# Performance work log

Measured on AMD Instinct MI355X. Metric: run time of the kernel, lower is better.

## Reference

```python
import jax, jax.numpy as jnp
import numpy as np
from jax import lax

B, S, T = 32, 128, 128
V_SRC, V_TGT, E, U = 32000, 32000, 128, 256


def _lstm(xs, h0, c0, Wx, Wh, b):
    # xs: [T, B, F]; Keras gate order i, f, g(candidate), o
    def step(carry, x):
        h, c = carry
        z = x @ Wx + h @ Wh + b
        i, f, g, o = jnp.split(z, 4, axis=-1)
        c = jax.nn.sigmoid(f) * c + jax.nn.sigmoid(i) * jnp.tanh(g)
        h = jax.nn.sigmoid(o) * jnp.tanh(c)
        return (h, c), h
    (h, c), hs = lax.scan(step, (h0, c0), xs)
    return hs, h, c


def setup_inputs() -> dict:
    key = jax.random.key(0)
    ks = jax.random.split(key, 20)
    p = lambda k, shp: (jax.random.normal(k, shp, dtype=jnp.float32) * 0.02)
    return {
        "src": jax.random.randint(ks[0], (B, S), 0, V_SRC),
        "tgt": jax.random.randint(ks[1], (B, T), 0, V_TGT),
        "enc_emb": p(ks[2], (V_SRC, E)),
        "enc_Wx": p(ks[3], (E, 4 * U)),
        "enc_Wh": p(ks[4], (U, 4 * U)),
        "enc_b": jnp.zeros((4 * U,), jnp.float32),
        "dec_emb": p(ks[5], (V_TGT, E)),
        "dec_Wx": p(ks[6], (U + E, 4 * U)),
        "dec_Wh": p(ks[7], (U, 4 * U)),
        "dec_b": jnp.zeros((4 * U,), jnp.float32),
        "att_W1": p(ks[8], (U, U)),
        "att_b1": jnp.zeros((U,), jnp.float32),
        "att_W2": p(ks[9], (U, U)),
        "att_b2": jnp.zeros((U,), jnp.float32),
        "att_V": p(ks[10], (U, 1)),
        "att_bV": jnp.zeros((1,), jnp.float32),
        "fc_W": p(ks[11], (U, V_TGT)),
        "fc_b": jnp.zeros((V_TGT,), jnp.float32),
    }


def reference(src, tgt, enc_emb, enc_Wx, enc_Wh, enc_b, dec_emb, dec_Wx, dec_Wh,
              dec_b, att_W1, att_b1, att_W2, att_b2, att_V, att_bV, fc_W, fc_b):
    # ---- encoder ----
    enc_x = enc_emb[src]                                  # [B,S,E]
    enc_hs, h, c = _lstm(enc_x.transpose(1, 0, 2),
                         jnp.zeros((B, U), enc_Wx.dtype),
                         jnp.zeros((B, U), enc_Wx.dtype),
                         enc_Wx, enc_Wh, enc_b)
    enc_out = enc_hs.transpose(1, 0, 2)                   # [B,S,U]
    keys = enc_out @ att_W2 + att_b2                      # [B,S,U] (hoisted, same math)

    # ---- decoder (faithful: step 0 uses tgt[:,0]; step t>=1 uses tgt[:,t-1]) ----
    dec_tokens = jnp.concatenate([tgt[:, :1], tgt[:, :-1]], axis=1)  # [B,T]
    dec_x = dec_emb[dec_tokens].transpose(1, 0, 2)        # [T,B,E]

    def step(carry, x_emb):
        h, c = carry
        q = (h @ att_W1 + att_b1)[:, None, :]             # [B,1,U]
        score = jnp.tanh(q + keys) @ att_V + att_bV       # [B,S,1]
        attn = jax.nn.softmax(score, axis=1)
        ctx = jnp.sum(attn * enc_out, axis=1)             # [B,U]
        xin = jnp.concatenate([ctx, x_emb], axis=-1)      # [B,U+E]
        z = xin @ dec_Wx + h @ dec_Wh + dec_b
        i, f, g, o = jnp.split(z, 4, axis=-1)
        c = jax.nn.sigmoid(f) * c + jax.nn.sigmoid(i) * jnp.tanh(g)
        h = jax.nn.sigmoid(o) * jnp.tanh(c)
        probs = jax.nn.softmax(h @ fc_W + fc_b, axis=-1)  # [B,V]
        return (h, c), probs

    _, out = lax.scan(step, (h, c), dec_x)                # [T,B,V]
    return out.transpose(1, 0, 2)                         # [B,T,V]
```

## Files before the change

kernel.cpp:

```cpp
#include <hip/hip_runtime.h>
#include <hip/hip_bf16.h>
#include <hip/hip_fp16.h>
#include <cstdint>
#include <cstddef>

#define B_ 32
#define S_ 128
#define T_ 128
#define E_ 128
#define U_ 256
#define V_ 32000
#define G4 1024
#define TV 4096000

typedef __attribute__((ext_vector_type(8))) short short8_t;
typedef __attribute__((ext_vector_type(8))) unsigned short ushort8_t;
typedef __attribute__((ext_vector_type(4))) float f32x4;
typedef unsigned long long u64;

static __device__ __forceinline__ unsigned short f2bf(float x) {
  union { float f; unsigned int u; } v; v.f = x;
  unsigned int r = (v.u + 0x7fffu + ((v.u >> 16) & 1u)) >> 16;
  return (unsigned short)r;
}
static __device__ __forceinline__ float bf2f(unsigned short u) {
  return __uint_as_float(((unsigned)u) << 16);
}
static __device__ __forceinline__ float sigmoidf_(float x) {
  return 1.0f / (1.0f + __expf(-x));
}
static __device__ __forceinline__ float tanhf_(float x) {
  float e = __expf(2.0f * x);
  return 1.0f - 2.0f / (e + 1.0f);
}

static __device__ __forceinline__ unsigned int f2e5(float x) {
  __half h = __float2half(x);
  __half_raw hr = *(__half_raw*)&h;
  unsigned int u = hr.x;
  unsigned int r = (u + 0x7Fu + ((u >> 8) & 1u)) >> 8;
  return r & 0xFFu;
}

static __device__ __forceinline__ unsigned pk2(float a, float b) {
  auto h = __builtin_amdgcn_cvt_pkrtz(a, b);
  return __builtin_bit_cast(unsigned, h);
}
#define SEL01 0x05000400u
#define SEL23 0x07000600u
static __device__ __forceinline__ unsigned e5pair(unsigned w, unsigned sel) {
  return __builtin_amdgcn_perm(w, 0u, sel);
}
static __device__ __forceinline__ float dot2(unsigned a, unsigned b, float c) {
  float d;
  asm("v_dot2_f32_f16 %0, %1, %2, %3" : "=v"(d) : "v"(a), "v"(b), "v"(c));
  return d;
}
static __device__ __forceinline__ unsigned pkadd(unsigned a, unsigned b) {
  unsigned d; asm("v_pk_add_f16 %0, %1, %2" : "=v"(d) : "v"(a), "v"(b)); return d;
}
static __device__ __forceinline__ unsigned pkmul(unsigned a, unsigned b) {
  unsigned d; asm("v_pk_mul_f16 %0, %1, %2" : "=v"(d) : "v"(a), "v"(b)); return d;
}
static __device__ __forceinline__ unsigned pkfma(unsigned a, unsigned b, unsigned c) {
  unsigned d; asm("v_pk_fma_f16 %0, %1, %2, %3" : "=v"(d) : "v"(a), "v"(b), "v"(c)); return d;
}
static __device__ __forceinline__ unsigned pkmax(unsigned a, unsigned b) {
  unsigned d; asm("v_pk_max_f16 %0, %1, %2" : "=v"(d) : "v"(a), "v"(b)); return d;
}
static __device__ __forceinline__ unsigned pkmin(unsigned a, unsigned b) {
  unsigned d; asm("v_pk_min_f16 %0, %1, %2" : "=v"(d) : "v"(a), "v"(b)); return d;
}

static __device__ __forceinline__ void gload_lds16(const void* g, void* l) {
  __builtin_amdgcn_global_load_lds(
      (const __attribute__((address_space(1))) unsigned int*)g,
      (__attribute__((address_space(3))) unsigned int*)l, 16, 0, 0);
}

static __device__ __forceinline__ void pub64u(u64* p, unsigned val, unsigned tag) {
  u64 v = ((u64)tag << 32) | (u64)val;
  __hip_atomic_store(p, v, __ATOMIC_RELAXED, __HIP_MEMORY_SCOPE_AGENT);
}
static __device__ __forceinline__ u64 ld64(const u64* p) {
  return __hip_atomic_load(p, __ATOMIC_RELAXED, __HIP_MEMORY_SCOPE_AGENT);
}

__global__ __launch_bounds__(256) void k_prep(
    const int* __restrict__ src, const int* __restrict__ tgt,
    const float* __restrict__ enc_emb, const float* __restrict__ enc_Wx,
    const float* __restrict__ enc_b,
    const float* __restrict__ dec_emb, const float* __restrict__ dec_Wx,
    const float* __restrict__ dec_b,
    float* __restrict__ Xe, float* __restrict__ Xd,
    const float* __restrict__ fcW, unsigned short* __restrict__ fcWt)
{
  __shared__ float shmem[64 * 65];
  int wg = blockIdx.x;
  int tid = threadIdx.x;

  if (wg >= 1024) {
    int bid = wg - 1024;
    int n0 = (bid % 500) * 64, k0 = (bid / 500) * 64;
    for (int i = 0; i < 16; ++i) {
      int lin = i * 256 + tid;
      int k = lin >> 6, n = lin & 63;
      shmem[k * 65 + n] = fcW[(size_t)(k0 + k) * V_ + n0 + n];
    }
    __syncthreads();
    for (int i = 0; i < 16; ++i) {
      int lin = i * 256 + tid;
      int n = lin >> 6, k = lin & 63;
      fcWt[(size_t)(n0 + n) * 256 + k0 + k] = f2bf(shmem[k * 65 + n]);
    }
    return;
  }

  bool is_dec = (wg >= 512);
  int r0 = (is_dec ? (wg - 512) : wg) * 8;
  const float* emb  = is_dec ? dec_emb : enc_emb;
  const float* W    = is_dec ? (dec_Wx + (size_t)U_ * G4) : enc_Wx;
  const float* bias = is_dec ? dec_b : enc_b;
  float* Xout = is_dec ? Xd : Xe;

  for (int i = 0; i < 4; ++i) {
    int lin = i * 256 + tid;
    int rr = lin >> 7, k = lin & 127;
    int r = r0 + rr;
    int b = r & 31, st = r >> 5;
    int tok;
// ... 90 lines not shown
      c_reg = c;
      float h = sigmoidf_(z[3]) * tanhf_(c);
      h_reg = h;
      enc_out[((size_t)(b * S_ + s)) * U_ + gc] = h;
      if (s < S_ - 1) {
        float hx = __shfl_xor(h, 1);
        if (!(r & 1))
          pub64u(&hpubE[((size_t)((s + 1) & 1) * 32 + b) * 128 + g * 16 + (r >> 1)],
                 pk2(h, hx), (unsigned)(s + 1));
      }
    }
    if (s < S_ - 1 && tid < 128) {
      const u64* p = &hpubE[((size_t)((s + 1) & 1) * 32 + b) * 128 + tid];
      u64 v = ld64(p);
      while ((unsigned)(v >> 32) < (unsigned)(s + 1)) { __builtin_amdgcn_s_sleep(1); v = ld64(p); }
      h2[tid] = (unsigned)v;
    }
    __syncthreads();
  }
  if (tid < 32) {
    h_state[b * U_ + g * 32 + tid] = h_reg;
    c_state[b * U_ + g * 32 + tid] = c_reg;
  }
}

__global__ __launch_bounds__(256) void k_keys(
    const float* __restrict__ enc_out, const float* __restrict__ W2,
    const float* __restrict__ b2,
    unsigned char* __restrict__ keys8, unsigned char* __restrict__ eo8T)
{
  __shared__ float x_l[8][U_];
  int wg = blockIdx.x, tid = threadIdx.x;
  int r0 = wg * 8;
  for (int i = 0; i < 8; ++i) x_l[i][tid] = enc_out[(size_t)(r0 + i) * U_ + tid];
  __syncthreads();
  float acc[8];
  #pragma unroll
  for (int rr = 0; rr < 8; ++rr) acc[rr] = 0.f;
  for (int k = 0; k < U_; ++k) {
    float w = W2[(size_t)k * U_ + tid];
    #pragma unroll
    for (int rr = 0; rr < 8; ++rr) acc[rr] += x_l[rr][k] * w;
  }
  float bb = b2[tid];
  #pragma unroll
  for (int rr = 0; rr < 8; ++rr) {
    int r = r0 + rr;
    keys8[(size_t)r * U_ + tid] = (unsigned char)f2e5(acc[rr] + bb);
    int bI = r >> 7, sI = r & 127;
    eo8T[((size_t)bI * U_ + tid) * S_ + sI] = (unsigned char)f2e5(x_l[rr][tid]);
  }
}

__global__ __launch_bounds__(1024) void k_decoder(
    const float* __restrict__ Xd, const float* __restrict__ dec_Wx,
    const float* __restrict__ Wh,
    const float* __restrict__ W1, const float* __restrict__ b1,
    const float* __restrict__ attV, const float* __restrict__ attbV,
    const unsigned char* __restrict__ keys8, const unsigned char* __restrict__ eo8T,
    const float* __restrict__ h0, const float* __restrict__ c0,
    unsigned short* __restrict__ Hbf,
    u64* __restrict__ hpub2 )
{
  __shared__ unsigned int WxU[64 * 128];
  __shared__ unsigned int WhU[64 * 128];
  __shared__ unsigned int W1U[64 * 256];
  __shared__ float scr_q[4 * 256];
  __shared__ float scr_c[4 * 256];
  __shared__ float scr_z[8 * 128];
  __shared__ unsigned int q2[160];
  __shared__ unsigned int aV2[160];
  __shared__ unsigned int h2[128];
  __shared__ unsigned int ctx2[128];
  __shared__ unsigned int esc2[64];
  __shared__ float escw[16];
  __shared__ float b1_l[256];

  int bid = blockIdx.x, tid = threadIdx.x;
  int b = bid & 31, g = bid >> 5;
  int lane = tid & 63, wid = tid >> 6;

  for (int idx = tid; idx < 64 * 128; idx += 1024) {
    int k4 = idx >> 7, c = idx & 127;
    int gc = (c >> 5) * 256 + g * 32 + (c & 31);
    unsigned wx = 0, wh = 0;
    #pragma unroll
    for (int i = 0; i < 4; ++i) {
      int k = 4 * k4 + i;
      wx |= f2e5(dec_Wx[(size_t)k * G4 + gc]) << (8 * i);
      wh |= f2e5(Wh[(size_t)k * G4 + gc]) << (8 * i);
    }
    WxU[k4 * 128 + c] = wx;
    WhU[k4 * 128 + c] = wh;
  }
  for (int idx = tid; idx < 64 * 256; idx += 1024) {
    int k4 = idx >> 8, u = idx & 255;
    unsigned w = 0;
    #pragma unroll
    for (int i = 0; i < 4; ++i)
      w |= f2e5(W1[(size_t)(4 * k4 + i) * U_ + u]) << (8 * i);
    W1U[k4 * 256 + u] = w;
  }
  if (tid < 128) {
    int p = tid;
    aV2[(p >> 4) * 20 + (p & 15)] = pk2(attV[2 * p], attV[2 * p + 1]);
  }
  if (tid < 256) b1_l[tid] = b1[tid];
  float bV = attbV[0];
  float c_reg = 0.f, h_reg = 0.f;
  if (tid < 32) {
    h_reg = h0[b * U_ + g * 32 + tid];
    c_reg = c0[b * U_ + g * 32 + tid];
  }
  __syncthreads();

  if (tid < 32) {
    float hx = __shfl_xor(h_reg, 1);
    if (!(tid & 1))
      pub64u(&hpub2[((size_t)0 * 32 + b) * 128 + g * 16 + (tid >> 1)], pk2(h_reg, hx), 1u);
  }
  if (tid < 128) {
    const u64* hp = &hpub2[((size_t)0 * 32 + b) * 128 + tid];
    u64 vh = ld64(hp);
    while ((unsigned)(vh >> 32) < 1u) { __builtin_amdgcn_s_sleep(1); vh = ld64(hp); }
    h2[tid] = (unsigned)vh;
  }
  __syncthreads();

  const unsigned NEG1 = pk2(-1.f, -1.f), POS1 = pk2(1.f, 1.f);
  const unsigned C1 = pk2(-0.333333333f, -0.333333333f);
  const unsigned C2 = pk2(0.133333333f, 0.133333333f);
  const unsigned C3 = pk2(-0.053968254f, -0.053968254f);

  const unsigned char* kb = keys8 + (size_t)b * S_ * U_;
  const unsigned char* eb = eo8T + (size_t)b * U_ * S_;

  for (int t = 0; t < T_; ++t) {
    float xd0 = 0.f, xd1 = 0.f, xd2 = 0.f, xd3 = 0.f;
    if (tid < 32) {
      const float* xd = Xd + (size_t)(t * B_ + b) * G4 + g * 32 + tid;
      xd0 = xd[0]; xd1 = xd[256]; xd2 = xd[512]; xd3 = xd[768];
    }

    int sI = tid >> 3, uo = tid & 7;
    int uI = tid & 255, sq = tid >> 8;
    uint4 kA, kB, eA, eB;
    {
      const uint4* kp = (const uint4*)(kb + (size_t)sI * U_ + uo * 32);
      kA = kp[0]; kB = kp[1];
      const uint4* ep = (const uint4*)(eb + (size_t)uI * S_ + sq * 32);
      eA = ep[0]; eB = ep[1];
    }
    {
      int c = tid & 255, kq = tid >> 8;
      const unsigned* wp = &W1U[(kq * 16) * 256 + c];
      const unsigned* hh = &h2[kq * 32];
      float qa = 0.f, qb = 0.f;
      #pragma unroll
      for (int j = 0; j < 16; ++j) {
        unsigned w = wp[j * 256];
        qa = dot2(e5pair(w, SEL01), hh[2 * j], qa);
        qb = dot2(e5pair(w, SEL23), hh[2 * j + 1], qb);
      }
      scr_q[kq * 256 + c] = qa + qb;
    }
    __syncthreads();

    if (tid < 128) {
      int u0 = 2 * tid;
      float q0 = scr_q[u0] + scr_q[256 + u0] + scr_q[512 + u0] + scr_q[768 + u0] + b1_l[u0];
      float q1 = scr_q[u0 + 1] + scr_q[256 + u0 + 1] + scr_q[512 + u0 + 1] + scr_q[768 + u0 + 1] + b1_l[u0 + 1];
      q2[(tid >> 4) * 20 + (tid & 15)] = pk2(q0, q1);
    }
    __syncthreads();

    {
      unsigned kw[8] = {kA.x, kA.y, kA.z, kA.w, kB.x, kB.y, kB.z, kB.w};
      const unsigned* qq = &q2[uo * 20];
      const unsigned* vv = &aV2[uo * 20];
      float a0 = 0.f, a1 = 0.f;
      #pragma unroll
      for (int j = 0; j < 8; ++j) {
        unsigned w = kw[j];
        unsigned x0 = pkadd(e5pair(w, SEL01), qq[2 * j]);
        unsigned x1 = pkadd(e5pair(w, SEL23), qq[2 * j + 1]);
        x0 = pkmin(pkmax(x0, NEG1), POS1);
        x1 = pkmin(pkmax(x1, NEG1), POS1);
        unsigned s0_ = pkmul(x0, x0), s1_ = pkmul(x1, x1);
        unsigned t0 = pkfma(s0_, C3, C2), t1 = pkfma(s1_, C3, C2);
        t0 = pkfma(s0_, t0, C1); t1 = pkfma(s1_, t1, C1);
        unsigned th0 = pkfma(pkmul(x0, s0_), t0, x0);
        unsigned th1 = pkfma(pkmul(x1, s1_), t1, x1);
        a0 = dot2(th0, vv[2 * j], a0);
        a1 = dot2(th1, vv[2 * j + 1], a1);
      }
      float a = a0 + a1;
      a += __shfl_xor(a, 1); a += __shfl_xor(a, 2); a += __shfl_xor(a, 4);
      float ea = __expf(a + bV);
      float ep = __shfl_xor(ea, 8);
      if (uo == 0 && !(sI & 1)) esc2[sI >> 1] = pk2(ea, ep);
      float dsum = ea;
      dsum += __shfl_xor(dsum, 8); dsum += __shfl_xor(dsum, 16); dsum += __shfl_xor(dsum, 32);
      if (lane == 0) escw[wid] = dsum;
    }
    __syncthreads();

    {
      unsigned ewv[8] = {eA.x, eA.y, eA.z, eA.w, eB.x, eB.y, eB.z, eB.w};
      const unsigned* e2 = &esc2[sq * 16];
      float c0a = 0.f, c1a = 0.f;
      #pragma unroll
      for (int j = 0; j < 8; ++j) {
        unsigned w = ewv[j];
        c0a = dot2(e5pair(w, SEL01), e2[2 * j], c0a);
        c1a = dot2(e5pair(w, SEL23), e2[2 * j + 1], c1a);
      }
      scr_c[sq * 256 + uI] = c0a + c1a;
    }
    __syncthreads();

    if (tid < 128) {
      int u0 = 2 * tid;
      float ca = scr_c[u0] + scr_c[256 + u0] + scr_c[512 + u0] + scr_c[768 + u0];
      float cb = scr_c[u0 + 1] + scr_c[256 + u0 + 1] + scr_c[512 + u0 + 1] + scr_c[768 + u0 + 1];
      ctx2[tid] = pk2(ca, cb);
    }
    __syncthreads();

    {
      float d = ((escw[0] + escw[1]) + (escw[2] + escw[3])) +
                ((escw[4] + escw[5]) + (escw[6] + escw[7])) +
                ((escw[8] + escw[9]) + (escw[10] + escw[11])) +
                ((escw[12] + escw[13]) + (escw[14] + escw[15]));
      float dinv = 1.0f / d;
      int c = tid & 127, k8 = tid >> 7;
      const unsigned* wxp = &WxU[(k8 * 8) * 128 + c];
      const unsigned* whp = &WhU[(k8 * 8) * 128 + c];
      const unsigned* cc = &ctx2[k8 * 16];
      const unsigned* hh = &h2[k8 * 16];
      float zx0 = 0.f, zx1 = 0.f, zh0 = 0.f, zh1 = 0.f;
      #pragma unroll
      for (int j = 0; j < 8; ++j) {
        unsigned wx = wxp[j * 128], wh = whp[j * 128];
        zx0 = dot2(e5pair(wx, SEL01), cc[2 * j], zx0);
        zx1 = dot2(e5pair(wx, SEL23), cc[2 * j + 1], zx1);
        zh0 = dot2(e5pair(wh, SEL01), hh[2 * j], zh0);
        zh1 = dot2(e5pair(wh, SEL23), hh[2 * j + 1], zh1);
      }
      scr_z[k8 * 128 + c] = (zh0 + zh1) + (zx0 + zx1) * dinv;
    }
    __syncthreads();

    if (tid < 32) {
      int r = tid, gc = g * 32 + r;
      float z[4] = {xd0, xd1, xd2, xd3};
      #pragma unroll
      for (int q = 0; q < 4; ++q) {
        int c = q * 32 + r;
        #pragma unroll
        for (int k8 = 0; k8 < 8; ++k8) z[q] += scr_z[k8 * 128 + c];
      }
      float c = sigmoidf_(z[1]) * c_reg + sigmoidf_(z[0]) * tanhf_(z[2]);
      c_reg = c;
      float h = sigmoidf_(z[3]) * tanhf_(c);
      h_reg = h;
      Hbf[(size_t)(t * B_ + b) * U_ + gc] = f2bf(h);
      if (t < T_ - 1) {
        int par1 = (t + 1) & 1;
        float hx = __shfl_xor(h, 1);
        if (!(r & 1))
          pub64u(&hpub2[((size_t)par1 * 32 + b) * 128 + g * 16 + (r >> 1)],
                 pk2(h, hx), (unsigned)(t + 2));
      }
    }
    if (t < T_ - 1 && tid < 128) {
      int par1 = (t + 1) & 1;
      unsigned tag2 = (unsigned)(t + 2);
      const u64* hp = &hpub2[((size_t)par1 * 32 + b) * 128 + tid];
      u64 vh = ld64(hp);
      while ((unsigned)(vh >> 32) < tag2) { __builtin_amdgcn_s_sleep(1); vh = ld64(hp); }
      h2[tid] = (unsigned)vh;
    }
    __syncthreads();
  }
}

__global__ __launch_bounds__(256) void k_fc(
    const unsigned short* __restrict__ Hbf, const unsigned short* __restrict__ fcWt,
    const float* __restrict__ fcb, float* __restrict__ out,
    unsigned short* __restrict__ expv,
    float* __restrict__ rs_part)
{
  __shared__ uint4 Al[128 * 8];
  __shared__ uint4 Bl[128 * 8];
  __shared__ float rsum_l[128][2];

  int bid = blockIdx.x, tid = threadIdx.x;
  int nt = bid >> 5, mt = bid & 31;
  int m0 = mt * 128, n0 = nt * 128;
  int lane = tid & 63, wave = tid >> 6;
  int wm = (wave >> 1) * 64, wn = (wave & 1) * 64;
  int g = lane >> 4, r15 = lane & 15;

  f32x4 acc[4][4];
  f32x4 zero = {0.f, 0.f, 0.f, 0.f};
  #pragma unroll
  for (int mi = 0; mi < 4; ++mi)
    #pragma unroll
    for (int ni = 0; ni < 4; ++ni) acc[mi][ni] = zero;

  const unsigned short* Ag = Hbf  + (size_t)m0 * 256;
  const unsigned short* Bg = fcWt + (size_t)n0 * 256;

  int lin0 = tid;
  for (int kt = 0; kt < 4; ++kt) {
    int kk = kt * 64;
    #pragma unroll
    for (int blk = 0; blk < 4; ++blk) {
      int lin = blk * 256 + lin0;
      int row = lin >> 3, kq = lin & 7;
      int kqs = kq ^ (row & 7);
      gload_lds16(Ag + (size_t)row * 256 + kk + kqs * 8,
                  &Al[blk * 256 + wave * 64]);
      gload_lds16(Bg + (size_t)row * 256 + kk + kqs * 8,
                  &Bl[blk * 256 + wave * 64]);
    }
    __syncthreads();
    #pragma unroll
    for (int kk2 = 0; kk2 < 2; ++kk2) {
      short8_t a[4], bfr[4];
      #pragma unroll
      for (int mi = 0; mi < 4; ++mi) {
        int row = wm + mi * 16 + r15;
        a[mi] = *(const short8_t*)&Al[row * 8 + ((kk2 * 4 + g) ^ (row & 7))];
      }
      #pragma unroll
      for (int ni = 0; ni < 4; ++ni) {
        int row = wn + ni * 16 + r15;
        bfr[ni] = *(const short8_t*)&Bl[row * 8 + ((kk2 * 4 + g) ^ (row & 7))];
      }
      #pragma unroll
      for (int mi = 0; mi < 4; ++mi)
        #pragma unroll
        for (int ni = 0; ni < 4; ++ni)
          acc[mi][ni] = __builtin_amdgcn_mfma_f32_16x16x32_bf16(a[mi], bfr[ni], acc[mi][ni], 0, 0, 0);
    }
    __syncthreads();
  }

  float fcb_l[4];
  #pragma unroll
  for (int ni = 0; ni < 4; ++ni) fcb_l[ni] = fcb[n0 + wn + ni * 16 + r15];

  #pragma unroll
  for (int mi = 0; mi < 4; ++mi) {
    #pragma unroll
    for (int jj = 0; jj < 4; ++jj) {
      int rloc = wm + mi * 16 + g * 4 + jj;
      int grow = m0 + rloc;
      int bb = grow & 31, tt = grow >> 5;
      size_t obase = (size_t)bb * TV + (size_t)tt * V_;
      float s = 0.f;
      if (expv) {
        #pragma unroll
        for (int ni = 0; ni < 4; ++ni) {
          float v = __expf(acc[mi][ni][jj] + fcb_l[ni]);
          unsigned short us = f2bf(v);
          expv[obase + n0 + wn + ni * 16 + r15] = us;
          s += bf2f(us);
        }
      } else {
        #pragma unroll
        for (int ni = 0; ni < 4; ++ni) {
          float v = __expf(acc[mi][ni][jj] + fcb_l[ni]);
          out[obase + n0 + wn + ni * 16 + r15] = v;
          s += v;
        }
      }
      s += __shfl_xor(s, 1); s += __shfl_xor(s, 2);
      s += __shfl_xor(s, 4); s += __shfl_xor(s, 8);
      if (r15 == 0) rsum_l[rloc][wave & 1] = s;
    }
  }
  __syncthreads();
  if (tid < 128)
    rs_part[(size_t)nt * 4096 + m0 + tid] = rsum_l[tid][0] + rsum_l[tid][1];
}

__global__ __launch_bounds__(256) void k_rowsum(
    const float* __restrict__ rs_part, float* __restrict__ row_inv)
{
  int gidx = blockIdx.x * 256 + threadIdx.x;
  float s = 0.f;
  for (int nt = 0; nt < 250; ++nt) s += rs_part[(size_t)nt * 4096 + gidx];
  row_inv[gidx] = 1.0f / s;
}

__global__ __launch_bounds__(256) void k_norm_bf16(
    const unsigned short* __restrict__ expv, float* __restrict__ out,
    const float* __restrict__ row_inv)
{
  const long total = 16384000;
  long stride = (long)gridDim.x * 256;
  for (long i = (long)blockIdx.x * 256 + threadIdx.x; i < total; i += stride) {
    long flat = i * 8;
    int bb = (int)(flat / TV);
    int rem = (int)(flat % TV);
    int tt = rem / V_;
    float sc = row_inv[tt * 32 + bb];
    ushort8_t v = *(const ushort8_t*)&expv[flat];
    float4 o0, o1;
    o0.x = bf2f(v[0]) * sc; o0.y = bf2f(v[1]) * sc;
    o0.z = bf2f(v[2]) * sc; o0.w = bf2f(v[3]) * sc;
    o1.x = bf2f(v[4]) * sc; o1.y = bf2f(v[5]) * sc;
    o1.z = bf2f(v[6]) * sc; o1.w = bf2f(v[7]) * sc;
    *(float4*)&out[flat] = o0;
    *(float4*)&out[flat + 4] = o1;
  }
}

__global__ __launch_bounds__(256) void k_norm(
    float4* __restrict__ out4, const float* __restrict__ row_inv)
{
  const long total = 32768000;
  long stride = (long)gridDim.x * 256;
  for (long i = (long)blockIdx.x * 256 + threadIdx.x; i < total; i += stride) {
    long flat = i * 4;
    int bb = (int)(flat / TV);
    int rem = (int)(flat % TV);
    int tt = rem / V_;
    float sc = row_inv[tt * 32 + bb];
    float4 v = out4[i];
    v.x *= sc; v.y *= sc; v.z *= sc; v.w *= sc;
    out4[i] = v;
  }
}

extern "C" void kernel_launch(void* const* d_in, const int* in_sizes, int n_in,
                              void* d_out, int out_size, void* d_ws, size_t ws_size,
                              hipStream_t stream) {
  (void)in_sizes; (void)n_in; (void)out_size;
  const int*   src     = (const int*)d_in[0];
  const int*   tgt     = (const int*)d_in[1];
  const float* enc_emb = (const float*)d_in[2];
  const float* enc_Wx  = (const float*)d_in[3];
  const float* enc_Wh  = (const float*)d_in[4];
  const float* enc_b   = (const float*)d_in[5];
  const float* dec_emb = (const float*)d_in[6];
  const float* dec_Wx  = (const float*)d_in[7];
  const float* dec_Wh  = (const float*)d_in[8];
  const float* dec_b   = (const float*)d_in[9];
  const float* att_W1  = (const float*)d_in[10];
  const float* att_b1  = (const float*)d_in[11];
  const float* att_W2  = (const float*)d_in[12];
  const float* att_b2  = (const float*)d_in[13];
  const float* att_V   = (const float*)d_in[14];
  const float* att_bV  = (const float*)d_in[15];
  const float* fc_W    = (const float*)d_in[16];
  const float* fc_b    = (const float*)d_in[17];
  float* out = (float*)d_out;

  char* ws = (char*)d_ws;
  size_t o = 0;
  auto alloc = [&](size_t bytes) {
    char* p = ws + o;
    o = (o + bytes + 255) & ~(size_t)255;
    return p;
  };
  float*          Xe      = (float*)alloc((size_t)S_ * B_ * G4 * 4);
  float*          Xd      = (float*)alloc((size_t)T_ * B_ * G4 * 4);
  float*          enc_out = (float*)alloc((size_t)B_ * S_ * U_ * 4);
  unsigned char*  keys8   = (unsigned char*)alloc((size_t)B_ * S_ * U_);
  unsigned char*  eo8T    = (unsigned char*)alloc((size_t)B_ * U_ * S_);
  unsigned short* Hbf     = (unsigned short*)alloc((size_t)T_ * B_ * U_ * 2);
  unsigned short* fcWt    = (unsigned short*)alloc((size_t)V_ * U_ * 2);
  float*          h_state = (float*)alloc((size_t)B_ * U_ * 4);
  float*          c_state = (float*)alloc((size_t)B_ * U_ * 4);
  float*          rs_part = (float*)alloc((size_t)250 * 4096 * 4);
  float*          row_inv = (float*)alloc((size_t)4096 * 4);
  size_t pub_off = o;
  u64* hpubE = (u64*)alloc((size_t)2 * 32 * 128 * 8);
  u64* hpub2 = (u64*)alloc((size_t)2 * 32 * 128 * 8);
  size_t pub_bytes = o - pub_off;
  size_t expv_bytes = (size_t)B_ * T_ * V_ * 2;
  unsigned short* expv = nullptr;
  if (o + expv_bytes <= ws_size)
    expv = (unsigned short*)alloc(expv_bytes);

  hipMemsetAsync(ws + pub_off, 0, pub_bytes, stream);
  hipLaunchKernelGGL(k_prep, dim3(3024), dim3(256), 0, stream,
                     src, tgt, enc_emb, enc_Wx, enc_b, dec_emb, dec_Wx, dec_b,
                     Xe, Xd, fc_W, fcWt);
  hipLaunchKernelGGL(k_encoder8, dim3(256), dim3(1024), 0, stream,
                     Xe, enc_Wh, enc_out, h_state, c_state, hpubE);
  hipLaunchKernelGGL(k_keys, dim3(512), dim3(256), 0, stream,
                     enc_out, att_W2, att_b2, keys8, eo8T);
  hipLaunchKernelGGL(k_decoder, dim3(256), dim3(1024), 0, stream,
                     Xd, dec_Wx, dec_Wh, att_W1, att_b1, att_V, att_bV,
                     keys8, eo8T, h_state, c_state, Hbf, hpub2);
  hipLaunchKernelGGL(k_fc, dim3(8000), dim3(256), 0, stream,
                     Hbf, fcWt, fc_b, out, expv, rs_part);
  hipLaunchKernelGGL(k_rowsum, dim3(16), dim3(256), 0, stream, rs_part, row_inv);
  if (expv)
    hipLaunchKernelGGL(k_norm_bf16, dim3(4096), dim3(256), 0, stream,
                       expv, out, row_inv);
  else
    hipLaunchKernelGGL(k_norm, dim3(2048), dim3(256), 0, stream,
                       (float4*)d_out, row_inv);
}
```

Baseline: 1.352 ms.

## Fuse decoder and FC into one persistent kernel overlapping vocab GEMM with recurrence

Merges the decoder recurrence and the vocabulary projection into one launch. 128 blocks run the decoder, now split across 4 gate groups of 64 units instead of 8 of 32, with the W1 query projection partitioned by k and published as partial sums through global flags. The other 128 blocks run the FC GEMM tiles, waiting on per-timestep counters so the vocab projection overlaps the sequential decoder. The costs are spin-waits and cross-block synchronisation that must be correct, and only half the grid doing FC work, which loses some FC parallelism compared with the old 8000-block launch.

```diff
diff --git a/kernel.cpp b/kernel.cpp
--- a/kernel.cpp
+++ b/kernel.cpp
@@ -16,6 +16,7 @@
 typedef __attribute__((ext_vector_type(8))) short short8_t;
 typedef __attribute__((ext_vector_type(8))) unsigned short ushort8_t;
 typedef __attribute__((ext_vector_type(4))) float f32x4;
+typedef __attribute__((ext_vector_type(4))) unsigned uint4v;
 typedef unsigned long long u64;
 
 static __device__ __forceinline__ unsigned short f2bf(float x) {
@@ -70,12 +71,6 @@
 }
 static __device__ __forceinline__ unsigned pkmin(unsigned a, unsigned b) {
   unsigned d; asm("v_pk_min_f16 %0, %1, %2" : "=v"(d) : "v"(a), "v"(b)); return d;
-}
-
-static __device__ __forceinline__ void gload_lds16(const void* g, void* l) {
-  __builtin_amdgcn_global_load_lds(
-      (const __attribute__((address_space(1))) unsigned int*)g,
-      (__attribute__((address_space(3))) unsigned int*)l, 16, 0, 0);
 }
 
 static __device__ __forceinline__ void pub64u(u64* p, unsigned val, unsigned tag) {
@@ -272,7 +267,29 @@
   }
 }
 
-__global__ __launch_bounds__(1024) void k_decoder(
+struct DecS {
+  unsigned WxU[64 * 256];
+  unsigned WhU[64 * 256];
+  unsigned W1U[16 * 256];
+  float scr_c[4 * 256];
+  float scr_z[4 * 256];
+  unsigned q2[160];
+  unsigned aV2[160];
+  unsigned b1p[128];
+  unsigned h2[128];
+  unsigned ctx2[128];
+  unsigned esc2[64];
+  float escw[16];
+  float hsl[64];
+};
+struct FcS {
+  uint4v Al[4][128 * 8];
+  uint4v Bl[4][128 * 8];
+  float rsum[4][128][2];
+};
+#define SMEM_MAX (sizeof(DecS) > sizeof(FcS) ? sizeof(DecS) : sizeof(FcS))
+
+__global__ __launch_bounds__(1024) void k_dec_fc(
     const float* __restrict__ Xd, const float* __restrict__ dec_Wx,
     const float* __restrict__ Wh,
     const float* __restrict__ W1, const float* __restrict__ b1,
@@ -280,331 +297,358 @@
     const unsigned char* __restrict__ keys8, const unsigned char* __restrict__ eo8T,
     const float* __restrict__ h0, const float* __restrict__ c0,
     unsigned short* __restrict__ Hbf,
-    u64* __restrict__ hpub2 )
+    u64* __restrict__ hpub2 ,
+    u64* __restrict__ qp2   ,
+    unsigned* __restrict__ cnt ,
+    const unsigned short* __restrict__ fcWt, const float* __restrict__ fcb,
+    float* __restrict__ out, unsigned short* __restrict__ expv,
+    float* __restrict__ rs_part)
 {
-  __shared__ unsigned int WxU[64 * 128];
-  __shared__ unsigned int WhU[64 * 128];
-  __shared__ unsigned int W1U[64 * 256];
-  __shared__ float scr_q[4 * 256];
-  __shared__ float scr_c[4 * 256];
-  __shared__ float scr_z[8 * 128];
-  __shared__ unsigned int q2[160];
-  __shared__ unsigned int aV2[160];
-  __shared__ unsigned int h2[128];
-  __shared__ unsigned int ctx2[128];
-  __shared__ unsigned int esc2[64];
-  __shared__ float escw[16];
-  __shared__ float b1_l[256];
-
+  __shared__ __align__(16) char smem_raw[SMEM_MAX];
   int bid = blockIdx.x, tid = threadIdx.x;
-  int b = bid & 31, g = bid >> 5;
-  int lane = tid & 63, wid = tid >> 6;
-
-  for (int idx = tid; idx < 64 * 128; idx += 1024) {
-    int k4 = idx >> 7, c = idx & 127;
-    int gc = (c >> 5) * 256 + g * 32 + (c & 31);
-    unsigned wx = 0, wh = 0;
-    #pragma unroll
-    for (int i = 0; i < 4; ++i) {
-      int k = 4 * k4 + i;
-      wx |= f2e5(dec_Wx[(size_t)k * G4 + gc]) << (8 * i);
-      wh |= f2e5(Wh[(size_t)k * G4 + gc]) << (8 * i);
-    }
-    WxU[k4 * 128 + c] = wx;
-    WhU[k4 * 128 + c] = wh;
-  }
-  for (int idx = tid; idx < 64 * 256; idx += 1024) {
-    int k4 = idx >> 8, u = idx & 255;
-    unsigned w = 0;
-    #pragma unroll
-    for (int i = 0; i < 4; ++i)
-      w |= f2e5(W1[(size_t)(4 * k4 + i) * U_ + u]) << (8 * i);
-    W1U[k4 * 256 + u] = w;
-  }
-  if (tid < 128) {
-    int p = tid;
-    aV2[(p >> 4) * 20 + (p & 15)] = pk2(attV[2 * p], attV[2 * p + 1]);
-  }
-  if (tid < 256) b1_l[tid] = b1[tid];
-  float bV = attbV[0];
-  float c_reg = 0.f, h_reg = 0.f;
-  if (tid < 32) {
-    h_reg = h0[b * U_ + g * 32 + tid];
-    c_reg = c0[b * U_ + g * 32 + tid];
-  }
-  __syncthreads();
-
-  if (tid < 32) {
-    float hx = __shfl_xor(h_reg, 1);
-    if (!(tid & 1))
-      pub64u(&hpub2[((size_t)0 * 32 + b) * 128 + g * 16 + (tid >> 1)], pk2(h_reg, hx), 1u);
-  }
-  if (tid < 128) {
-    const u64* hp = &hpub2[((size_t)0 * 32 + b) * 128 + tid];
-    u64 vh = ld64(hp);
-    while ((unsigned)(vh >> 32) < 1u) { __builtin_amdgcn_s_sleep(1); vh = ld64(hp); }
-    h2[tid] = (unsigned)vh;
-  }
-  __syncthreads();
-
-  const unsigned NEG1 = pk2(-1.f, -1.f), POS1 = pk2(1.f, 1.f);
-  const unsigned C1 = pk2(-0.333333333f, -0.333333333f);
-  const unsigned C2 = pk2(0.133333333f, 0.133333333f);
-  const unsigned C3 = pk2(-0.053968254f, -0.053968254f);
-
-  const unsigned char* kb = keys8 + (size_t)b * S_ * U_;
-  const unsigned char* eb = eo8T + (size_t)b * U_ * S_;
-
-  for (int t = 0; t < T_; ++t) {
-    float xd0 = 0.f, xd1 = 0.f, xd2 = 0.f, xd3 = 0.f;
-    if (tid < 32) {
-      const float* xd = Xd + (size_t)(t * B_ + b) * G4 + g * 32 + tid;
-      xd0 = xd[0]; xd1 = xd[256]; xd2 = xd[512]; xd3 = xd[768];
-    }
-
-    int sI = tid >> 3, uo = tid & 7;
-    int uI = tid & 255, sq = tid >> 8;
-    uint4 kA, kB, eA, eB;
-    {
-      const uint4* kp = (const uint4*)(kb + (size_t)sI * U_ + uo * 32);
-      kA = kp[0]; kB = kp[1];
-      const uint4* ep = (const uint4*)(eb + (size_t)uI * S_ + sq * 32);
-      eA = ep[0]; eB = ep[1];
-    }
-    {
-      int c = tid & 255, kq = tid >> 8;
-      const unsigned* wp = &W1U[(kq * 16) * 256 + c];
-      const unsigned* hh = &h2[kq * 32];
+
+  if (bid < 128) {
+    DecS& S = *(DecS*)smem_raw;
+    int b = bid & 31, g = bid >> 5;
+    int lane = tid & 63, wid = tid >> 6;
+
+    for (int idx = tid; idx < 64 * 256; idx += 1024) {
+      int k4 = idx >> 8, c = idx & 255;
+      int gc = (c >> 6) * 256 + g * 64 + (c & 63);
+      unsigned wx = 0, wh = 0;
+      #pragma unroll
+      for (int i = 0; i < 4; ++i) {
+        int k = 4 * k4 + i;
+        wx |= f2e5(dec_Wx[(size_t)k * G4 + gc]) << (8 * i);
+        wh |= f2e5(Wh[(size_t)k * G4 + gc]) << (8 * i);
+      }
+      S.WxU[k4 * 256 + c] = wx;
+      S.WhU[k4 * 256 + c] = wh;
+    }
+    for (int idx = tid; idx < 16 * 256; idx += 1024) {
+      int k4 = idx >> 8, u = idx & 255;
+      unsigned w = 0;
+      #pragma unroll
+      for (int i = 0; i < 4; ++i)
+        w |= f2e5(W1[(size_t)(g * 64 + 4 * k4 + i) * U_ + u]) << (8 * i);
+      S.W1U[k4 * 256 + u] = w;
+    }
+    if (tid < 128) {
+      S.aV2[(tid >> 4) * 20 + (tid & 15)] = pk2(attV[2 * tid], attV[2 * tid + 1]);
+      S.b1p[tid] = pk2(b1[2 * tid], b1[2 * tid + 1]);
+    }
+    float bV = attbV[0];
+    float c_reg = 0.f, h_reg = 0.f;
+    if (tid < 64) {
+      h_reg = h0[b * U_ + g * 64 + tid];
+      c_reg = c0[b * U_ + g * 64 + tid];
+      S.hsl[tid] = h_reg;
+    }
+    __syncthreads();
+
+    if (tid < 256) {
       float qa = 0.f, qb = 0.f;
       #pragma unroll
       for (int j = 0; j < 16; ++j) {
-        unsigned w = wp[j * 256];
-        qa = dot2(e5pair(w, SEL01), hh[2 * j], qa);
-        qb = dot2(e5pair(w, SEL23), hh[2 * j + 1], qb);
-      }
-      scr_q[kq * 256 + c] = qa + qb;
-    }
-    __syncthreads();
-
-    if (tid < 128) {
-      int u0 = 2 * tid;
-      float q0 = scr_q[u0] + scr_q[256 + u0] + scr_q[512 + u0] + scr_q[768 + u0] + b1_l[u0];
-      float q1 = scr_q[u0 + 1] + scr_q[256 + u0 + 1] + scr_q[512 + u0 + 1] + scr_q[768 + u0 + 1] + b1_l[u0 + 1];
-      q2[(tid >> 4) * 20 + (tid & 15)] = pk2(q0, q1);
-    }
-    __syncthreads();
-
-    {
-      unsigned kw[8] = {kA.x, kA.y, kA.z, kA.w, kB.x, kB.y, kB.z, kB.w};
-      const unsigned* qq = &q2[uo * 20];
-      const unsigned* vv = &aV2[uo * 20];
-      float a0 = 0.f, a1 = 0.f;
-      #pragma unroll
-      for (int j = 0; j < 8; ++j) {
-        unsigned w = kw[j];
-        unsigned x0 = pkadd(e5pair(w, SEL01), qq[2 * j]);
-        unsigned x1 = pkadd(e5pair(w, SEL23), qq[2 * j + 1]);
-        x0 = pkmin(pkmax(x0, NEG1), POS1);
-        x1 = pkmin(pkmax(x1, NEG1), POS1);
-        unsigned s0_ = pkmul(x0, x0), s1_ = pkmul(x1, x1);
-        unsigned t0 = pkfma(s0_, C3, C2), t1 = pkfma(s1_, C3, C2);
-        t0 = pkfma(s0_, t0, C1); t1 = pkfma(s1_, t1, C1);
-        unsigned th0 = pkfma(pkmul(x0, s0_), t0, x0);
-        unsigned th1 = pkfma(pkmul(x1, s1_), t1, x1);
-        a0 = dot2(th0, vv[2 * j], a0);
-        a1 = dot2(th1, vv[2 * j + 1], a1);
-      }
-      float a = a0 + a1;
-      a += __shfl_xor(a, 1); a += __shfl_xor(a, 2); a += __shfl_xor(a, 4);
-      float ea = __expf(a + bV);
-      float ep = __shfl_xor(ea, 8);
-      if (uo == 0 && !(sI & 1)) esc2[sI >> 1] = pk2(ea, ep);
-      float dsum = ea;
-      dsum += __shfl_xor(dsum, 8); dsum += __shfl_xor(dsum, 16); dsum += __shfl_xor(dsum, 32);
-      if (lane == 0) escw[wid] = dsum;
-    }
-    __syncthreads();
-
-    {
-      unsigned ewv[8] = {eA.x, eA.y, eA.z, eA.w, eB.x, eB.y, eB.z, eB.w};
-      const unsigned* e2 = &esc2[sq * 16];
-      float c0a = 0.f, c1a = 0.f;
-      #pragma unroll
-      for (int j = 0; j < 8; ++j) {
-        unsigned w = ewv[j];
-        c0a = dot2(e5pair(w, SEL01), e2[2 * j], c0a);
-        c1a = dot2(e5pair(w, SEL23), e2[2 * j + 1], c1a);
-      }
-      scr_c[sq * 256 + uI] = c0a + c1a;
-    }
-    __syncthreads();
-
-    if (tid < 128) {
-      int u0 = 2 * tid;
-      float ca = scr_c[u0] + scr_c[256 + u0] + scr_c[512 + u0] + scr_c[768 + u0];
-      float cb = scr_c[u0 + 1] + scr_c[256 + u0 + 1] + scr_c[512 + u0 + 1] + scr_c[768 + u0 + 1];
-      ctx2[tid] = pk2(ca, cb);
-    }
-    __syncthreads();
-
-    {
-      float d = ((escw[0] + escw[1]) + (escw[2] + escw[3])) +
-                ((escw[4] + escw[5]) + (escw[6] + escw[7])) +
-                ((escw[8] + escw[9]) + (escw[10] + escw[11])) +
-                ((escw[12] + escw[13]) + (escw[14] + escw[15]));
-      float dinv = 1.0f / d;
-      int c = tid & 127, k8 = tid >> 7;
-      const unsigned* wxp = &WxU[(k8 * 8) * 128 + c];
-      const unsigned* whp = &WhU[(k8 * 8) * 128 + c];
-      const unsigned* cc = &ctx2[k8 * 16];
-      const unsigned* hh = &h2[k8 * 16];
-      float zx0 = 0.f, zx1 = 0.f, zh0 = 0.f, zh1 = 0.f;
-      #pragma unroll
-      for (int j = 0; j < 8; ++j) {
-        unsigned wx = wxp[j * 128], wh = whp[j * 128];
-        zx0 = dot2(e5pair(wx, SEL01), cc[2 * j], zx0);
-        zx1 = dot2(e5pair(wx, SEL23), cc[2 * j + 1], zx1);
-        zh0 = dot2(e5pair(wh, SEL01), hh[2 * j], zh0);
-        zh1 = dot2(e5pair(wh, SEL23), hh[2 * j + 1], zh1);
-      }
-      scr_z[k8 * 128 + c] = (zh0 + zh1) + (zx0 + zx1) * dinv;
-    }
-    __syncthreads();
-
-    if (tid < 32) {
-      int r = tid, gc = g * 32 + r;
-      float z[4] = {xd0, xd1, xd2, xd3};
-      #pragma unroll
-      for (int q = 0; q < 4; ++q) {
-        int c = q * 32 + r;
-        #pragma unroll
-        for (int k8 = 0; k8 < 8; ++k8) z[q] += scr_z[k8 * 128 + c];
-      }
-      float c = sigmoidf_(z[1]) * c_reg + sigmoidf_(z[0]) * tanhf_(z[2]);
-      c_reg = c;
-      float h = sigmoidf_(z[3]) * tanhf_(c);
-      h_reg = h;
-      Hbf[(size_t)(t * B_ + b) * U_ + gc] = f2bf(h);
-      if (t < T_ - 1) {
-        int par1 = (t + 1) & 1;
-        float hx = __shfl_xor(h, 1);
-        if (!(r & 1))
-          pub64u(&hpub2[((size_t)par1 * 32 + b) * 128 + g * 16 + (r >> 1)],
-                 pk2(h, hx), (unsigned)(t + 2));
-      }
-    }
-    if (t < T_ - 1 && tid < 128) {
+        unsigned w = S.W1U[j * 256 + tid];
+        qa = dot2(e5pair(w, SEL01), pk2(S.hsl[4 * j],     S.hsl[4 * j + 1]), qa);
+        qb = dot2(e5pair(w, SEL23), pk2(S.hsl[4 * j + 2], S.hsl[4 * j + 3]), qb);
+      }
+      float qp = qa + qb;
+      float qpx = __shfl_xor(qp, 1);
+      if (!(tid & 1))
+        pub64u(&qp2[(((size_t)0 * 32 + b) * 128 + (tid >> 1)) * 4 + g], pk2(qp, qpx), 1u);
+    }
+    if (tid < 64) {
+      float hx = __shfl_xor(h_reg, 1);
+      if (!(tid & 1))
+        pub64u(&hpub2[((size_t)0 * 32 + b) * 128 + g * 32 + (tid >> 1)], pk2(h_reg, hx), 1u);
+    }
+
+    const unsigned NEG1 = pk2(-1.f, -1.f), POS1 = pk2(1.f, 1.f);
+    const unsigned C1 = pk2(-0.333333333f, -0.333333333f);
+    const unsigned C2 = pk2(0.133333333f, 0.133333333f);
+    const unsigned C3 = pk2(-0.053968254f, -0.053968254f);
+
+    const unsigned char* kb = keys8 + (size_t)b * S_ * U_;
+    const unsigned char* eb = eo8T + (size_t)b * U_ * S_;
+
+    for (int t = 0; t < T_; ++t) {
+      unsigned tag = (unsigned)(t + 1);
+      int par = t & 1;
+
+      float xd0 = 0.f, xd1 = 0.f, xd2 = 0.f, xd3 = 0.f;
+      if (tid < 64) {
+        const float* xd = Xd + (size_t)(t * B_ + b) * G4 + g * 64 + tid;
+        xd0 = xd[0]; xd1 = xd[256]; xd2 = xd[512]; xd3 = xd[768];
+      }
+
+      if (tid < 128) {
+        const u64* hp = &hpub2[((size_t)par * 32 + b) * 128 + tid];
+        const u64* qp = &qp2[(((size_t)par * 32 + b) * 128 + tid) * 4];
+        u64 vh, v0, v1, v2, v3;
+        bool ok;
+        do {
+          vh = ld64(hp);
+          v0 = ld64(qp); v1 = ld64(qp + 1); v2 = ld64(qp + 2); v3 = ld64(qp + 3);
+          ok = ((unsigned)(vh >> 32) >= tag) & ((unsigned)(v0 >> 32) >= tag) &
+               ((unsigned)(v1 >> 32) >= tag) & ((unsigned)(v2 >> 32) >= tag) &
+               ((unsigned)(v3 >> 32) >= tag);
+          if (!ok) __builtin_amdgcn_s_sleep(1);
+        } while (!ok);
+        S.h2[tid] = (unsigned)vh;
+        unsigned qs = pkadd(pkadd((unsigned)v0, (unsigned)v1),
+                            pkadd((unsigned)v2, (unsigned)v3));
+        S.q2[(tid >> 4) * 20 + (tid & 15)] = pkadd(qs, S.b1p[tid]);
+      }
+      __syncthreads();
+
+      int sI = tid >> 3, uo = tid & 7;
+      int uI = tid & 255, sq = tid >> 8;
+      uint4v kw0, kw1, ew0, ew1;
+      {
+        const uint4v* kp = (const uint4v*)(kb + (size_t)sI * U_ + uo * 32);
+        kw0 = kp[0]; kw1 = kp[1];
+        const uint4v* ep = (const uint4v*)(eb + (size_t)uI * S_ + sq * 32);
+        ew0 = ep[0]; ew1 = ep[1];
+      }
+      float zreg;
+      {
+        int c = tid & 255, kq = tid >> 8;
+        const unsigned* wp = &S.WhU[(kq * 16) * 256 + c];
+        const unsigned* hh = &S.h2[kq * 32];
+        float z0 = 0.f, z1 = 0.f;
+        #pragma unroll
+        for (int j = 0; j < 16; ++j) {
+          unsigned w = wp[j * 256];
+          z0 = dot2(e5pair(w, SEL01), hh[2 * j], z0);
+          z1 = dot2(e5pair(w, SEL23), hh[2 * j + 1], z1);
+        }
+        zreg = z0 + z1;
+      }
+      {
+        unsigned kw[8] = {kw0.x, kw0.y, kw0.z, kw0.w, kw1.x, kw1.y, kw1.z, kw1.w};
+        const unsigned* qq = &S.q2[uo * 20];
+        const unsigned* vv = &S.aV2[uo * 20];
+        float a0 = 0.f, a1 = 0.f;
+        #pragma unroll
+        for (int j = 0; j < 8; ++j) {
+          unsigned w = kw[j];
+          unsigned x0 = pkadd(e5pair(w, SEL01), qq[2 * j]);
+          unsigned x1 = pkadd(e5pair(w, SEL23), qq[2 * j + 1]);
+          x0 = pkmin(pkmax(x0, NEG1), POS1);
+          x1 = pkmin(pkmax(x1, NEG1), POS1);
+          unsigned s0_ = pkmul(x0, x0), s1_ = pkmul(x1, x1);
+          unsigned t0 = pkfma(s0_, C3, C2), t1 = pkfma(s1_, C3, C2);
+          t0 = pkfma(s0_, t0, C1); t1 = pkfma(s1_, t1, C1);
+          unsigned th0 = pkfma(pkmul(x0, s0_), t0, x0);
+          unsigned th1 = pkfma(pkmul(x1, s1_), t1, x1);
+          a0 = dot2(th0, vv[2 * j], a0);
+          a1 = dot2(th1, vv[2 * j + 1], a1);
+        }
+        float a = a0 + a1;
+        a += __shfl_xor(a, 1); a += __shfl_xor(a, 2); a += __shfl_xor(a, 4);
+        float ea = __expf(a + bV);
+        float ep = __shfl_xor(ea, 8);
+        if (uo == 0 && !(sI & 1)) S.esc2[sI >> 1] = pk2(ea, ep);
+        float dsum = ea;
+        dsum += __shfl_xor(dsum, 8); dsum += __shfl_xor(dsum, 16); dsum += __shfl_xor(dsum, 32);
+        if (lane == 0) S.escw[wid] = dsum;
+      }
+      __syncthreads();
+
+      {
+        unsigned ewv[8] = {ew0.x, ew0.y, ew0.z, ew0.w, ew1.x, ew1.y, ew1.z, ew1.w};
+        const unsigned* e2 = &S.esc2[sq * 16];
+        float c0a = 0.f, c1a = 0.f;
+        #pragma unroll
+        for (int j = 0; j < 8; ++j) {
+          unsigned w = ewv[j];
+          c0a = dot2(e5pair(w, SEL01), e2[2 * j], c0a);
+          c1a = dot2(e5pair(w, SEL23), e2[2 * j + 1], c1a);
+        }
+        S.scr_c[sq * 256 + uI] = c0a + c1a;
+      }
+      __syncthreads();
+
+      if (tid < 128) {
+        float d = ((S.escw[0] + S.escw[1]) + (S.escw[2] + S.escw[3])) +
+                  ((S.escw[4] + S.escw[5]) + (S.escw[6] + S.escw[7])) +
+                  ((S.escw[8] + S.escw[9]) + (S.escw[10] + S.escw[11])) +
+                  ((S.escw[12] + S.escw[13]) + (S.escw[14] + S.escw[15]));
+        float dinv = 1.0f / d;
+        int u0 = 2 * tid;
+        float ca = (S.scr_c[u0] + S.scr_c[256 + u0] + S.scr_c[512 + u0] + S.scr_c[768 + u0]) * dinv;
+        float cb = (S.scr_c[u0 + 1] + S.scr_c[256 + u0 + 1] + S.scr_c[512 + u0 + 1] + S.scr_c[768 + u0 + 1]) * dinv;
+        S.ctx2[tid] = pk2(ca, cb);
+      }
+      __syncthreads();
+
+      {
+        int c = tid & 255, kq = tid >> 8;
+        const unsigned* wp = &S.WxU[(kq * 16) * 256 + c];
+        const unsigned* cc = &S.ctx2[kq * 32];
+        float z0 = 0.f, z1 = 0.f;
+        #pragma unroll
+        for (int j = 0; j < 16; ++j) {
+          unsigned w = wp[j * 256];
+          z0 = dot2(e5pair(w, SEL01), cc[2 * j], z0);
+          z1 = dot2(e5pair(w, SEL23), cc[2 * j + 1], z1);
+        }
+        S.scr_z[kq * 256 + c] = zreg + z0 + z1;
+      }
+      __syncthreads();
+
       int par1 = (t + 1) & 1;
       unsigned tag2 = (unsigned)(t + 2);
-      const u64* hp = &hpub2[((size_t)par1 * 32 + b) * 128 + tid];
-      u64 vh = ld64(hp);
-      while ((unsigned)(vh >> 32) < tag2) { __builtin_amdgcn_s_sleep(1); vh = ld64(hp); }
-      h2[tid] = (unsigned)vh;
+      if (tid < 64) {
+        int r = tid, gc = g * 64 + r;
+        float z[4];
+        #pragma unroll
+        for (int q = 0; q < 4; ++q) {
+          int c = q * 64 + r;
+          z[q] = S.scr_z[c] + S.scr_z[256 + c] + S.scr_z[512 + c] + S.scr_z[768 + c];
+        }
+        z[0] += xd0; z[1] += xd1; z[2] += xd2; z[3] += xd3;
+        float c = sigmoidf_(z[1]) * c_reg + sigmoidf_(z[0]) * tanhf_(z[2]);
+        c_reg = c;
+        float h = sigmoidf_(z[3]) * tanhf_(c);
+        h_reg = h;
+        S.hsl[r] = h;
+        Hbf[(size_t)(t * B_ + b) * U_ + gc] = f2bf(h);
+        if (t < T_ - 1) {
+          float hx = __shfl_xor(h, 1);
+          if (!(r & 1))
+            pub64u(&hpub2[((size_t)par1 * 32 + b) * 128 + g * 32 + (r >> 1)], pk2(h, hx), tag2);
+        }
+      }
+      if (tid == 0)
+        __hip_atomic_fetch_add(&cnt[t], 1u, __ATOMIC_RELEASE, __HIP_MEMORY_SCOPE_AGENT);
+      __syncthreads();
+
+      if (t < T_ - 1 && tid < 256) {
+        float qa = 0.f, qb = 0.f;
+        #pragma unroll
+        for (int j = 0; j < 16; ++j) {
+          unsigned w = S.W1U[j * 256 + tid];
+          qa = dot2(e5pair(w, SEL01), pk2(S.hsl[4 * j],     S.hsl[4 * j + 1]), qa);
+          qb = dot2(e5pair(w, SEL23), pk2(S.hsl[4 * j + 2], S.hsl[4 * j + 3]), qb);
+        }
+        float qp = qa + qb;
+        float qpx = __shfl_xor(qp, 1);
+        if (!(tid & 1))
+          pub64u(&qp2[(((size_t)par1 * 32 + b) * 128 + (tid >> 1)) * 4 + g], pk2(qp, qpx), tag2);
+      }
+    }
+    return;
+  }
+
+  FcS& F = *(FcS*)smem_raw;
+  int w = bid - 128;
+  int stid = tid & 255, sub = tid >> 8;
+  int lane = tid & 63, wv = (tid >> 6) & 3;
+  int wm = (wv >> 1) * 64, wn = (wv & 1) * 64;
+  int gq = lane >> 4, r15 = lane & 15;
+
+  for (int i = 0; i < 16; ++i) {
+    int t4 = i * 512 + w * 4;
+    if (t4 >= 8000) break;
+    int tile = t4 + sub;
+    int mt = tile / 250, nt = tile % 250;
+    int m0 = mt * 128, n0 = nt * 128;
+
+    if (tid == 0) {
+      int mtmax = (t4 + 3) / 250;
+      while (__hip_atomic_load(&cnt[4 * mtmax + 3], __ATOMIC_RELAXED,
+                               __HIP_MEMORY_SCOPE_AGENT) < 128u)
+        __builtin_amdgcn_s_sleep(16);
     }
     __syncthreads();
-  }
-}
-
-__global__ __launch_bounds__(256) void k_fc(
-    const unsigned short* __restrict__ Hbf, const unsigned short* __restrict__ fcWt,
-    const float* __restrict__ fcb, float* __restrict__ out,
-    unsigned short* __restrict__ expv,
-    float* __restrict__ rs_part)
-{
-  __shared__ uint4 Al[128 * 8];
-  __shared__ uint4 Bl[128 * 8];
-  __shared__ float rsum_l[128][2];
-
-  int bid = blockIdx.x, tid = threadIdx.x;
-  int nt = bid >> 5, mt = bid & 31;
-  int m0 = mt * 128, n0 = nt * 128;
-  int lane = tid & 63, wave = tid >> 6;
-  int wm = (wave >> 1) * 64, wn = (wave & 1) * 64;
-  int g = lane >> 4, r15 = lane & 15;
-
-  f32x4 acc[4][4];
-  f32x4 zero = {0.f, 0.f, 0.f, 0.f};
-  #pragma unroll
-  for (int mi = 0; mi < 4; ++mi)
+
+    f32x4 acc[4][4];
+    f32x4 zero = {0.f, 0.f, 0.f, 0.f};
     #pragma unroll
-    for (int ni = 0; ni < 4; ++ni) acc[mi][ni] = zero;
-
-  const unsigned short* Ag = Hbf  + (size_t)m0 * 256;
-  const unsigned short* Bg = fcWt + (size_t)n0 * 256;
-
-  int lin0 = tid;
-  for (int kt = 0; kt < 4; ++kt) {
-    int kk = kt * 64;
+    for (int mi = 0; mi < 4; ++mi)
+      #pragma unroll
+      for (int ni = 0; ni < 4; ++ni) acc[mi][ni] = zero;
+
+    const unsigned short* Ag = Hbf  + (size_t)m0 * 256;
+    const unsigned short* Bg = fcWt + (size_t)n0 * 256;
+
+    for (int kt = 0; kt < 4; ++kt) {
+      int kk = kt * 64;
+      #pragma unroll
+      for (int blk = 0; blk < 4; ++blk) {
+        int lin = blk * 256 + stid;
+        int row = lin >> 3, kq = lin & 7;
+        int slot = row * 8 + (kq ^ (row & 7));
+        F.Al[sub][slot] = __builtin_nontemporal_load(
+            (const uint4v*)(Ag + (size_t)row * 256 + kk + kq * 8));
+        F.Bl[sub][slot] = *(const uint4v*)(Bg + (size_t)row * 256 + kk + kq * 8);
+      }
+      __syncthreads();
+      #pragma unroll
+      for (int kk2 = 0; kk2 < 2; ++kk2) {
+        short8_t a[4], bfr[4];
+        #pragma unroll
+        for (int mi = 0; mi < 4; ++mi) {
+          int row = wm + mi * 16 + r15;
+          a[mi] = *(const short8_t*)&F.Al[sub][row * 8 + ((kk2 * 4 + gq) ^ (row & 7))];
+        }
+        #pragma unroll
+        for (int ni = 0; ni < 4; ++ni) {
+          int row = wn + ni * 16 + r15;
+          bfr[ni] = *(const short8_t*)&F.Bl[sub][row * 8 + ((kk2 * 4 + gq) ^ (row & 7))];
+        }
+        #pragma unroll
+        for (int mi = 0; mi < 4; ++mi)
+          #pragma unroll
+          for (int ni = 0; ni < 4; ++ni)
+            acc[mi][ni] = __builtin_amdgcn_mfma_f32_16x16x32_bf16(a[mi], bfr[ni], acc[mi][ni], 0, 0, 0);
+      }
+      __syncthreads();
+    }
+
+    float fcb_l[4];
     #pragma unroll
-    for (int blk = 0; blk < 4; ++blk) {
-      int lin = blk * 256 + lin0;
-      int row = lin >> 3, kq = lin & 7;
-      int kqs = kq ^ (row & 7);
-      gload_lds16(Ag + (size_t)row * 256 + kk + kqs * 8,
-                  &Al[blk * 256 + wave * 64]);
-      gload_lds16(Bg + (size_t)row * 256 + kk + kqs * 8,
-                  &Bl[blk * 256 + wave * 64]);
+    for (int ni = 0; ni < 4; ++ni) fcb_l[ni] = fcb[n0 + wn + ni * 16 + r15];
+
+    #pragma unroll
+    for (int mi = 0; mi < 4; ++mi) {
+      #pragma unroll
+      for (int jj = 0; jj < 4; ++jj) {
+        int rloc = wm + mi * 16 + gq * 4 + jj;
+        int grow = m0 + rloc;
+        int bb = grow & 31, tt = grow >> 5;
+        size_t obase = (size_t)bb * TV + (size_t)tt * V_;
+        float s = 0.f;
+        if (expv) {
+          #pragma unroll
+          for (int ni = 0; ni < 4; ++ni) {
+            float v = __expf(acc[mi][ni][jj] + fcb_l[ni]);
+            unsigned short us = f2bf(v);
+            expv[obase + n0 + wn + ni * 16 + r15] = us;
+            s += bf2f(us);
+          }
+        } else {
+          #pragma unroll
+          for (int ni = 0; ni < 4; ++ni) {
+            float v = __expf(acc[mi][ni][jj] + fcb_l[ni]);
+            out[obase + n0 + wn + ni * 16 + r15] = v;
+            s += v;
+          }
+        }
+        s += __shfl_xor(s, 1); s += __shfl_xor(s, 2);
+        s += __shfl_xor(s, 4); s += __shfl_xor(s, 8);
+        if (r15 == 0) F.rsum[sub][rloc][wv & 1] = s;
+      }
     }
     __syncthreads();
-    #pragma unroll
-    for (int kk2 = 0; kk2 < 2; ++kk2) {
-      short8_t a[4], bfr[4];
-      #pragma unroll
-      for (int mi = 0; mi < 4; ++mi) {
-        int row = wm + mi * 16 + r15;
-        a[mi] = *(const short8_t*)&Al[row * 8 + ((kk2 * 4 + g) ^ (row & 7))];
-      }
-      #pragma unroll
-      for (int ni = 0; ni < 4; ++ni) {
-        int row = wn + ni * 16 + r15;
-        bfr[ni] = *(const short8_t*)&Bl[row * 8 + ((kk2 * 4 + g) ^ (row & 7))];
-      }
-      #pragma unroll
-      for (int mi = 0; mi < 4; ++mi)
-        #pragma unroll
-        for (int ni = 0; ni < 4; ++ni)
-          acc[mi][ni] = __builtin_amdgcn_mfma_f32_16x16x32_bf16(a[mi], bfr[ni], acc[mi][ni], 0, 0, 0);
-    }
+    if (stid < 128)
+      rs_part[(size_t)nt * 4096 + m0 + stid] =
+          F.rsum[sub][stid][0] + F.rsum[sub][stid][1];
     __syncthreads();
   }
-
-  float fcb_l[4];
-  #pragma unroll
-  for (int ni = 0; ni < 4; ++ni) fcb_l[ni] = fcb[n0 + wn + ni * 16 + r15];
-
-  #pragma unroll
-  for (int mi = 0; mi < 4; ++mi) {
-    #pragma unroll
-    for (int jj = 0; jj < 4; ++jj) {
-      int rloc = wm + mi * 16 + g * 4 + jj;
-      int grow = m0 + rloc;
-      int bb = grow & 31, tt = grow >> 5;
-      size_t obase = (size_t)bb * TV + (size_t)tt * V_;
-      float s = 0.f;
-      if (expv) {
-        #pragma unroll
-        for (int ni = 0; ni < 4; ++ni) {
-          float v = __expf(acc[mi][ni][jj] + fcb_l[ni]);
-          unsigned short us = f2bf(v);
-          expv[obase + n0 + wn + ni * 16 + r15] = us;
-          s += bf2f(us);
-        }
-      } else {
-        #pragma unroll
-        for (int ni = 0; ni < 4; ++ni) {
-          float v = __expf(acc[mi][ni][jj] + fcb_l[ni]);
-          out[obase + n0 + wn + ni * 16 + r15] = v;
-          s += v;
-        }
-      }
-      s += __shfl_xor(s, 1); s += __shfl_xor(s, 2);
-      s += __shfl_xor(s, 4); s += __shfl_xor(s, 8);
-      if (r15 == 0) rsum_l[rloc][wave & 1] = s;
-    }
-  }
-  __syncthreads();
-  if (tid < 128)
-    rs_part[(size_t)nt * 4096 + m0 + tid] = rsum_l[tid][0] + rsum_l[tid][1];
 }
 
 __global__ __launch_bounds__(256) void k_rowsum(
@@ -699,15 +743,17 @@
   float*          rs_part = (float*)alloc((size_t)250 * 4096 * 4);
   float*          row_inv = (float*)alloc((size_t)4096 * 4);
   size_t pub_off = o;
-  u64* hpubE = (u64*)alloc((size_t)2 * 32 * 128 * 8);
-  u64* hpub2 = (u64*)alloc((size_t)2 * 32 * 128 * 8);
+  u64*      hpubE = (u64*)alloc((size_t)2 * 32 * 128 * 8);
+  u64*      hpub2 = (u64*)alloc((size_t)2 * 32 * 128 * 8);
+  u64*      qp2   = (u64*)alloc((size_t)2 * 32 * 128 * 4 * 8);
+  unsigned* cnt   = (unsigned*)alloc((size_t)128 * 4);
   size_t pub_bytes = o - pub_off;
   size_t expv_bytes = (size_t)B_ * T_ * V_ * 2;
   unsigned short* expv = nullptr;
   if (o + expv_bytes <= ws_size)
     expv = (unsigned short*)alloc(expv_bytes);
 
-  hipMemsetAsync(ws + pub_off, 0, pub_bytes, stream);
+  (void)hipMemsetAsync(ws + pub_off, 0, pub_bytes, stream);
   hipLaunchKernelGGL(k_prep, dim3(3024), dim3(256), 0, stream,
                      src, tgt, enc_emb, enc_Wx, enc_b, dec_emb, dec_Wx, dec_b,
                      Xe, Xd, fc_W, fcWt);
@@ -715,11 +761,10 @@
                      Xe, enc_Wh, enc_out, h_state, c_state, hpubE);
   hipLaunchKernelGGL(k_keys, dim3(512), dim3(256), 0, stream,
                      enc_out, att_W2, att_b2, keys8, eo8T);
-  hipLaunchKernelGGL(k_decoder, dim3(256), dim3(1024), 0, stream,
+  hipLaunchKernelGGL(k_dec_fc, dim3(256), dim3(1024), 0, stream,
                      Xd, dec_Wx, dec_Wh, att_W1, att_b1, att_V, att_bV,
-                     keys8, eo8T, h_state, c_state, Hbf, hpub2);
-  hipLaunchKernelGGL(k_fc, dim3(8000), dim3(256), 0, stream,
-                     Hbf, fcWt, fc_b, out, expv, rs_part);
+                     keys8, eo8T, h_state, c_state, Hbf, hpub2, qp2, cnt,
+                     fcWt, fc_b, out, expv, rs_part);
   hipLaunchKernelGGL(k_rowsum, dim3(16), dim3(256), 0, stream, rs_part, row_inv);
   if (expv)
     hipLaunchKernelGGL(k_norm_bf16, dim3(4096), dim3(256), 0, stream,
```

After: 1.763 ms. +30.5%, slower.
